# Kernel tuning notes

Measured on AMD Instinct MI355X. Metric: run time of the kernel, lower is better.

## Reference

```python
import jax, jax.numpy as jnp
import numpy as np

B, H, SQ, SKV, D = 4, 16, 1024, 1024, 64


def setup_inputs() -> dict:
    key = jax.random.key(0)
    k1, k2, k3, k4, k5 = jax.random.split(key, 5)
    return {
        "query": jax.random.normal(k1, (B, H, SQ, D), dtype=jnp.float32),
        "keys": jax.random.normal(k2, (B, H, SKV, D), dtype=jnp.float32),
        "values": jax.random.normal(k3, (B, H, SKV, D), dtype=jnp.float32),
        "mask": jax.random.randint(k4, (B, 1, SQ, SKV), 0, 2, dtype=jnp.int32),
        "additional_logits": jax.random.normal(k5, (B, H, SQ, SKV), dtype=jnp.float32),
    }


def reference(query, keys, values, mask, additional_logits):
    # logits = Q K^T + additional_logits, scaled by sqrt(d)
    logits = jnp.einsum("bhqd,bhkd->bhqk", query, keys)
    logits = logits + additional_logits
    logits = logits / jnp.sqrt(jnp.asarray(query.shape[-1], logits.dtype))
    # masked_fill(mask == 0, -1000.0); mask broadcasts over heads
    logits = jnp.where(mask == 0, jnp.asarray(-1000.0, logits.dtype), logits)
    weights = jax.nn.softmax(logits, axis=-1)
    context_vector = jnp.einsum("bhqk,bhkd->bhqd", weights, values)
    return context_vector, weights
```

## Files before the change

kernel.cpp:

```cpp
#include <hip/hip_runtime.h>

#define NB 4
#define NH 16
#define NSQ 1024
#define NSKV 1024
#define ND 64

typedef __attribute__((ext_vector_type(8))) short short8;
typedef __attribute__((ext_vector_type(4))) float f32x4;
typedef __attribute__((ext_vector_type(4))) int int4v;
typedef __attribute__((ext_vector_type(4))) unsigned int uint4v;
typedef __attribute__((ext_vector_type(2))) unsigned int uint2v;

__device__ __forceinline__ unsigned int cvt_pk(float lo, float hi) {
  unsigned int r;
  asm("v_cvt_pk_bf16_f32 %0, %1, %2" : "=v"(r) : "v"(lo), "v"(hi));
  return r;
}
__device__ __forceinline__ unsigned short f2bf(float f) {
  unsigned int u = __float_as_uint(f);
  u += 0x7FFFu + ((u >> 16) & 1u);
  return (unsigned short)(u >> 16);
}
__device__ __forceinline__ float bf2f(unsigned short h) {
  return __uint_as_float(((unsigned int)h) << 16);
}
__device__ __forceinline__ void bar() { __builtin_amdgcn_s_barrier(); }
__device__ __forceinline__ void lgkm0() {
  asm volatile("s_waitcnt lgkmcnt(0)" ::: "memory");
}

__global__ __launch_bounds__(512, 2)
void attn_fused(const float* __restrict__ Q, const float* __restrict__ K,
                const float* __restrict__ V, const int* __restrict__ M,
                const float* __restrict__ A, float* __restrict__ Octx,
                float* __restrict__ Ow)
{
  __shared__ unsigned short Ps[64 * 1024];
  __shared__ __align__(16) unsigned char Stg[18432];
  __shared__ float SumS[64][2];

  const int t  = threadIdx.x;
  const int w  = t >> 6;
  const int l  = t & 63;
  const int lg = l >> 4;
  const int lm = l & 15;
  const int p  = w & 3;
  const int h  = w >> 2;
  const int g  = p * 64 + l;

  const int bid = blockIdx.x;
  const int qt  = bid & 15;
  const int bh  = bid >> 4;
  const int b   = bh >> 4;
  const int q0  = qt * 64;
  const int qw  = q0 + p * 16;
  const int kvb = h * 512;

  const float* Qp = Q + (size_t)bh * NSQ * ND;
  const float* Kp = K + (size_t)bh * NSKV * ND;
  const float* Vp = V + (size_t)bh * NSKV * ND;
  const float* Ap = A + (size_t)bh * NSQ * NSKV;
  const int*   Mp = M + (size_t)b  * NSQ * NSKV;

  unsigned char* KsB = Stg + h * 4096;
  unsigned char* VtB = Stg + 8192 + h * 5120;

  const float C = 0.18033688011112042f;

  short8 qf[2];
  {
    const float* qr = Qp + (size_t)(qw + lm) * ND + lg * 8;
    #pragma unroll
    for (int dc = 0; dc < 2; ++dc) {
      f32x4 x = *(const f32x4*)(qr + dc * 32);
      f32x4 y = *(const f32x4*)(qr + dc * 32 + 4);
      uint4v u;
      u[0] = cvt_pk(x[0], x[1]); u[1] = cvt_pk(x[2], x[3]);
      u[2] = cvt_pk(y[0], y[1]); u[3] = cvt_pk(y[2], y[3]);
      qf[dc] = __builtin_bit_cast(short8, u);
    }
  }

  f32x4 ctx[4];
  #pragma unroll
  for (int i = 0; i < 4; ++i) ctx[i] = (f32x4){0.f, 0.f, 0.f, 0.f};
  float sum = 0.f;

  f32x4 aA[2], aB[2];  int4v mA[2], mB[2];
  f32x4 skA[2], svA[2], skB[2], svB[2];

  auto loadAM = [&](int kv0, f32x4* a, int4v* m) {
    #pragma unroll
    for (int sub = 0; sub < 2; ++sub) {
      size_t off = (size_t)(qw + lm) * NSKV + (kv0 + sub * 16 + lg * 4);
      a[sub] = *(const f32x4*)(Ap + off);
      m[sub] = *(const int4v*)(Mp + off);
    }
  };
  auto issueStage = [&](int kv0, f32x4* sk, f32x4* sv) {
    const float* kb = Kp + (size_t)kv0 * ND;
    const float* vb = Vp + (size_t)kv0 * ND;
    sk[0] = *(const f32x4*)(kb + g * 4);
    sk[1] = *(const f32x4*)(kb + 1024 + g * 4);
    sv[0] = *(const f32x4*)(vb + g * 4);
    sv[1] = *(const f32x4*)(vb + 1024 + g * 4);
  };
  auto writeStage = [&](const f32x4* sk, const f32x4* sv) {
    #pragma unroll
    for (int i = 0; i < 2; ++i) {
      int f = g * 4 + i * 1024;
      int row = f >> 6;
      int cb  = (f & 63) * 2;
      uint2v u;
      u[0] = cvt_pk(sk[i][0], sk[i][1]);
      u[1] = cvt_pk(sk[i][2], sk[i][3]);
      *(uint2v*)(KsB + row * 128 + (cb ^ ((row & 7) << 4))) = u;
      int kv = row, d0 = f & 63;
      #pragma unroll
      for (int j = 0; j < 4; ++j) {
        int d = d0 + j;
        *(unsigned short*)(VtB + d * 80 + ((kv * 2) ^ (((d >> 2) & 3) << 4))) =
            f2bf(sv[i][j]);
      }
    }
  };

  auto chunk = [&](int kv0, const f32x4* a, const int4v* m) {
    const int ksw = (lm & 7) << 4;
    const int vsw = ((lm >> 2) & 3) << 4;
    short8 kf[4];
    #pragma unroll
    for (int sub = 0; sub < 2; ++sub)
      #pragma unroll
      for (int dc = 0; dc < 2; ++dc)
        kf[sub * 2 + dc] = *(const short8*)(
            KsB + (sub * 16 + lm) * 128 + ((dc * 64 + lg * 16) ^ ksw));
    short8 vf[4];
    #pragma unroll
    for (int ds = 0; ds < 4; ++ds)
      vf[ds] = *(const short8*)(VtB + (ds * 16 + lm) * 80 + ((lg * 16) ^ vsw));

    #pragma unroll
    for (int sub = 0; sub < 2; ++sub) {
      f32x4 acc = (f32x4){0.f, 0.f, 0.f, 0.f};
      #pragma unroll
      for (int dc = 0; dc < 2; ++dc)
        acc = __builtin_amdgcn_mfma_f32_16x16x32_bf16(kf[sub * 2 + dc], qf[dc],
                                                      acc, 0, 0, 0);
      float pe[4];
      #pragma unroll
      for (int j = 0; j < 4; ++j) {
        float amc = m[sub][j] ? a[sub][j] * C : -1.8e8f;
        pe[j] = exp2f(fmaf(acc[j], C, amc));
        sum += pe[j];
      }
      uint2v u2;
      u2[0] = cvt_pk(pe[0], pe[1]); u2[1] = cvt_pk(pe[2], pe[3]);
      int colb = (kv0 + sub * 16 + lg * 4) * 2;
      *(uint2v*)((char*)Ps + (p * 16 + lm) * 2048 + (colb ^ (lm << 4))) = u2;
    }
    lgkm0();
    __builtin_amdgcn_sched_barrier(0);
    short8 pf = *(const short8*)((const char*)Ps + (p * 16 + lm) * 2048 +
                                 (((kv0 + lg * 8) * 2) ^ (lm << 4)));
    #pragma unroll
    for (int ds = 0; ds < 4; ++ds)
      ctx[ds] = __builtin_amdgcn_mfma_f32_16x16x32_bf16(pf, vf[ds], ctx[ds], 0, 0, 0);
  };

  issueStage(kvb, skA, svA);
  loadAM(kvb, aA, mA);
  for (int c = 0; c < 16; c += 2) {
    int kv0 = kvb + c * 32;
    bar();
    writeStage(skA, svA);
    issueStage(kv0 + 32, skB, svB);
    loadAM(kv0 + 32, aB, mB);
    lgkm0(); bar();
    chunk(kv0, aA, mA);
    bar();
    writeStage(skB, svB);
    if (c < 14) { issueStage(kv0 + 64, skA, svA); loadAM(kv0 + 64, aA, mA); }
    lgkm0(); bar();
    chunk(kv0 + 32, aB, mB);
  }

  sum += __shfl_xor(sum, 16);
  sum += __shfl_xor(sum, 32);
  if (lg == 0) SumS[p * 16 + lm][h] = sum;
  lgkm0(); bar();

  float (*CtxS)[16][64] = (float(*)[16][64])Stg;
  if (h == 1) {
    #pragma unroll
    for (int ds = 0; ds < 4; ++ds)
      #pragma unroll
      for (int j = 0; j < 4; ++j)
        CtxS[p][lg * 4 + j][ds * 16 + lm] = ctx[ds][j];
  }
  lgkm0(); bar();

  if (h == 0) {
    float rcpj[4];
    #pragma unroll
    for (int j = 0; j < 4; ++j) {
      int r = p * 16 + lg * 4 + j;
      rcpj[j] = 1.0f / (SumS[r][0] + SumS[r][1]);
    }
    #pragma unroll
    for (int ds = 0; ds < 4; ++ds)
      #pragma unroll
      for (int j = 0; j < 4; ++j)
        Octx[((size_t)bh * NSQ + qw + lg * 4 + j) * ND + ds * 16 + lm] =
            (ctx[ds][j] + CtxS[p][lg * 4 + j][ds * 16 + lm]) * rcpj[j];
  }

  float* Owp = Ow + (size_t)bh * NSQ * NSKV + (size_t)qw * NSKV;
  for (int r = 0; r < 16; ++r) {
    float rr = 1.0f / (SumS[p * 16 + r][0] + SumS[p * 16 + r][1]);
    int kv = kvb + l * 8;
    short8 pv = *(const short8*)((const char*)Ps + (p * 16 + r) * 2048 +
                                 ((kv * 2) ^ (r << 4)));
    f32x4 o1, o2;
    o1[0] = bf2f((unsigned short)pv[0]) * rr;
    o1[1] = bf2f((unsigned short)pv[1]) * rr;
    o1[2] = bf2f((unsigned short)pv[2]) * rr;
    o1[3] = bf2f((unsigned short)pv[3]) * rr;
    o2[0] = bf2f((unsigned short)pv[4]) * rr;
    o2[1] = bf2f((unsigned short)pv[5]) * rr;
    o2[2] = bf2f((unsigned short)pv[6]) * rr;
    o2[3] = bf2f((unsigned short)pv[7]) * rr;
    *(f32x4*)&Owp[(size_t)r * NSKV + kv]     = o1;
    *(f32x4*)&Owp[(size_t)r * NSKV + kv + 4] = o2;
  }
}

extern "C" void kernel_launch(void* const* d_in, const int* in_sizes, int n_in,
                              void* d_out, int out_size, void* d_ws, size_t ws_size,
                              hipStream_t stream) {
  const float* Q = (const float*)d_in[0];
  const float* K = (const float*)d_in[1];
  const float* V = (const float*)d_in[2];
  const int*   M = (const int*)d_in[3];
  const float* A = (const float*)d_in[4];
  float* ctx = (float*)d_out;
  float* wts = ctx + (size_t)NB * NH * NSQ * ND;
  dim3 grid(NB * NH * (NSQ / 64));
  attn_fused<<<grid, dim3(512), 0, stream>>>(Q, K, V, M, A, ctx, wts);
}
```

Measured before the change: 205.9 us.

## Split work into 16-row blocks with per-wave private KV staging and quarter KV ranges

Each block now handles 16 query rows with 4 waves, and each wave owns a quarter of the KV range. Every wave stages its own K/V tiles in private LDS, so the main loop needs no block-wide barriers. Shared LDS per block drops sharply, allowing more blocks per CU, and a bid remap interleaves heads. In exchange every K/V tile is reloaded for each 16-row block, four times as often as before, and the partial contexts from four waves must be reduced.

Measured after the change: 243.2 us. 1.18x slower.

```diff
diff --git a/kernel.cpp b/kernel.cpp
--- a/kernel.cpp
+++ b/kernel.cpp
@@ -7,6 +7,7 @@
 #define ND 64
 
 typedef __attribute__((ext_vector_type(8))) short short8;
+typedef __attribute__((ext_vector_type(4))) short short4v;
 typedef __attribute__((ext_vector_type(4))) float f32x4;
 typedef __attribute__((ext_vector_type(4))) int int4v;
 typedef __attribute__((ext_vector_type(4))) unsigned int uint4v;
@@ -25,37 +26,33 @@
 __device__ __forceinline__ float bf2f(unsigned short h) {
   return __uint_as_float(((unsigned int)h) << 16);
 }
-__device__ __forceinline__ void bar() { __builtin_amdgcn_s_barrier(); }
 __device__ __forceinline__ void lgkm0() {
   asm volatile("s_waitcnt lgkmcnt(0)" ::: "memory");
 }
 
-__global__ __launch_bounds__(512, 2)
+__global__ __launch_bounds__(256, 2)
 void attn_fused(const float* __restrict__ Q, const float* __restrict__ K,
                 const float* __restrict__ V, const int* __restrict__ M,
                 const float* __restrict__ A, float* __restrict__ Octx,
                 float* __restrict__ Ow)
 {
-  __shared__ unsigned short Ps[64 * 1024];
-  __shared__ __align__(16) unsigned char Stg[18432];
-  __shared__ float SumS[64][2];
+  __shared__ unsigned short Ps[16 * 1024];
+  __shared__ __align__(16) unsigned short Ks[4][32 * 64];
+  __shared__ __align__(16) unsigned short Vt[4][64 * 40];
+  __shared__ float SumS[16][4];
 
   const int t  = threadIdx.x;
   const int w  = t >> 6;
   const int l  = t & 63;
   const int lg = l >> 4;
   const int lm = l & 15;
-  const int p  = w & 3;
-  const int h  = w >> 2;
-  const int g  = p * 64 + l;
 
   const int bid = blockIdx.x;
-  const int qt  = bid & 15;
-  const int bh  = bid >> 4;
+  const int bh  = (bid & 7) + ((bid >> 9) << 3);
+  const int qt  = (bid >> 3) & 63;
   const int b   = bh >> 4;
-  const int q0  = qt * 64;
-  const int qw  = q0 + p * 16;
-  const int kvb = h * 512;
+  const int q0  = qt * 16;
+  const int kvq = w * 256;
 
   const float* Qp = Q + (size_t)bh * NSQ * ND;
   const float* Kp = K + (size_t)bh * NSKV * ND;
@@ -63,14 +60,14 @@
   const float* Ap = A + (size_t)bh * NSQ * NSKV;
   const int*   Mp = M + (size_t)b  * NSQ * NSKV;
 
-  unsigned char* KsB = Stg + h * 4096;
-  unsigned char* VtB = Stg + 8192 + h * 5120;
+  unsigned short* Ksw = Ks[w];
+  unsigned short* Vtw = Vt[w];
 
   const float C = 0.18033688011112042f;
 
   short8 qf[2];
   {
-    const float* qr = Qp + (size_t)(qw + lm) * ND + lg * 8;
+    const float* qr = Qp + (size_t)(q0 + lm) * ND + lg * 8;
     #pragma unroll
     for (int dc = 0; dc < 2; ++dc) {
       f32x4 x = *(const f32x4*)(qr + dc * 32);
@@ -87,46 +84,43 @@
   for (int i = 0; i < 4; ++i) ctx[i] = (f32x4){0.f, 0.f, 0.f, 0.f};
   float sum = 0.f;
 
+  f32x4 sk[8], sv[8];
   f32x4 aA[2], aB[2];  int4v mA[2], mB[2];
-  f32x4 skA[2], svA[2], skB[2], svB[2];
-
+
+  auto issueStage = [&](int kv0) {
+    const float* kb = Kp + (size_t)kv0 * ND + l * 4;
+    const float* vb = Vp + (size_t)kv0 * ND + l * 4;
+    #pragma unroll
+    for (int i = 0; i < 8; ++i) {
+      sk[i] = *(const f32x4*)(kb + i * 256);
+      sv[i] = *(const f32x4*)(vb + i * 256);
+    }
+  };
   auto loadAM = [&](int kv0, f32x4* a, int4v* m) {
     #pragma unroll
     for (int sub = 0; sub < 2; ++sub) {
-      size_t off = (size_t)(qw + lm) * NSKV + (kv0 + sub * 16 + lg * 4);
+      size_t off = (size_t)(q0 + lm) * NSKV + kv0 + sub * 16 + lg * 4;
       a[sub] = *(const f32x4*)(Ap + off);
       m[sub] = *(const int4v*)(Mp + off);
     }
   };
-  auto issueStage = [&](int kv0, f32x4* sk, f32x4* sv) {
-    const float* kb = Kp + (size_t)kv0 * ND;
-    const float* vb = Vp + (size_t)kv0 * ND;
-    sk[0] = *(const f32x4*)(kb + g * 4);
-    sk[1] = *(const f32x4*)(kb + 1024 + g * 4);
-    sv[0] = *(const f32x4*)(vb + g * 4);
-    sv[1] = *(const f32x4*)(vb + 1024 + g * 4);
-  };
-  auto writeStage = [&](const f32x4* sk, const f32x4* sv) {
-    #pragma unroll
-    for (int i = 0; i < 2; ++i) {
-      int f = g * 4 + i * 1024;
-      int row = f >> 6;
-      int cb  = (f & 63) * 2;
-      uint2v u;
-      u[0] = cvt_pk(sk[i][0], sk[i][1]);
-      u[1] = cvt_pk(sk[i][2], sk[i][3]);
-      *(uint2v*)(KsB + row * 128 + (cb ^ ((row & 7) << 4))) = u;
-      int kv = row, d0 = f & 63;
+  auto writeStage = [&]() {
+    #pragma unroll
+    for (int i = 0; i < 8; ++i) {
+      int row = i * 4 + (l >> 4);
+      uint2v ku;
+      ku[0] = cvt_pk(sk[i][0], sk[i][1]); ku[1] = cvt_pk(sk[i][2], sk[i][3]);
+      *(uint2v*)((char*)Ksw + row * 128 + (((l & 15) * 8) ^ ((row & 7) << 4))) = ku;
       #pragma unroll
       for (int j = 0; j < 4; ++j) {
-        int d = d0 + j;
-        *(unsigned short*)(VtB + d * 80 + ((kv * 2) ^ (((d >> 2) & 3) << 4))) =
-            f2bf(sv[i][j]);
+        int d = (l & 15) * 4 + j;
+        *(unsigned short*)((char*)Vtw + d * 80 +
+                           ((row * 2) ^ (((d >> 2) & 3) << 4))) = f2bf(sv[i][j]);
       }
     }
   };
 
-  auto chunk = [&](int kv0, const f32x4* a, const int4v* m) {
+  auto compute = [&](int kv0, const f32x4* a, const int4v* m) {
     const int ksw = (lm & 7) << 4;
     const int vsw = ((lm >> 2) & 3) << 4;
     short8 kf[4];
@@ -135,11 +129,12 @@
       #pragma unroll
       for (int dc = 0; dc < 2; ++dc)
         kf[sub * 2 + dc] = *(const short8*)(
-            KsB + (sub * 16 + lm) * 128 + ((dc * 64 + lg * 16) ^ ksw));
+            (const char*)Ksw + (sub * 16 + lm) * 128 + ((dc * 64 + lg * 16) ^ ksw));
     short8 vf[4];
     #pragma unroll
     for (int ds = 0; ds < 4; ++ds)
-      vf[ds] = *(const short8*)(VtB + (ds * 16 + lm) * 80 + ((lg * 16) ^ vsw));
+      vf[ds] = *(const short8*)(
+          (const char*)Vtw + (ds * 16 + lm) * 80 + ((lg * 16) ^ vsw));
 
     #pragma unroll
     for (int sub = 0; sub < 2; ++sub) {
@@ -157,82 +152,77 @@
       }
       uint2v u2;
       u2[0] = cvt_pk(pe[0], pe[1]); u2[1] = cvt_pk(pe[2], pe[3]);
-      int colb = (kv0 + sub * 16 + lg * 4) * 2;
-      *(uint2v*)((char*)Ps + (p * 16 + lm) * 2048 + (colb ^ (lm << 4))) = u2;
+      *(uint2v*)((char*)Ps + lm * 2048 +
+                 (((kv0 + sub * 16 + lg * 4) * 2) ^ (lm << 4))) = u2;
     }
     lgkm0();
     __builtin_amdgcn_sched_barrier(0);
-    short8 pf = *(const short8*)((const char*)Ps + (p * 16 + lm) * 2048 +
+    short8 pf = *(const short8*)((const char*)Ps + lm * 2048 +
                                  (((kv0 + lg * 8) * 2) ^ (lm << 4)));
     #pragma unroll
     for (int ds = 0; ds < 4; ++ds)
       ctx[ds] = __builtin_amdgcn_mfma_f32_16x16x32_bf16(pf, vf[ds], ctx[ds], 0, 0, 0);
   };
 
-  issueStage(kvb, skA, svA);
-  loadAM(kvb, aA, mA);
-  for (int c = 0; c < 16; c += 2) {
-    int kv0 = kvb + c * 32;
-    bar();
-    writeStage(skA, svA);
-    issueStage(kv0 + 32, skB, svB);
-    loadAM(kv0 + 32, aB, mB);
-    lgkm0(); bar();
-    chunk(kv0, aA, mA);
-    bar();
-    writeStage(skB, svB);
-    if (c < 14) { issueStage(kv0 + 64, skA, svA); loadAM(kv0 + 64, aA, mA); }
-    lgkm0(); bar();
-    chunk(kv0 + 32, aB, mB);
+  issueStage(kvq);
+  loadAM(kvq, aA, mA);
+  for (int c = 0; c < 8; c += 2) {
+    int kv0 = kvq + c * 32;
+    loadAM(kvq + ((c + 1) & 7) * 32, aB, mB);
+    writeStage();
+    issueStage(kvq + ((c + 1) & 7) * 32);
+    lgkm0();
+    compute(kv0, aA, mA);
+    loadAM(kvq + ((c + 2) & 7) * 32, aA, mA);
+    writeStage();
+    issueStage(kvq + ((c + 2) & 7) * 32);
+    lgkm0();
+    compute(kv0 + 32, aB, mB);
   }
 
   sum += __shfl_xor(sum, 16);
   sum += __shfl_xor(sum, 32);
-  if (lg == 0) SumS[p * 16 + lm][h] = sum;
-  lgkm0(); bar();
-
-  float (*CtxS)[16][64] = (float(*)[16][64])Stg;
-  if (h == 1) {
+  if (l < 16) SumS[l][w] = sum;
+  __syncthreads();
+
+  float (*CtxS)[16][64] = (float(*)[16][64])(&Ks[0][0]);
+  if (w) {
     #pragma unroll
     for (int ds = 0; ds < 4; ++ds)
       #pragma unroll
       for (int j = 0; j < 4; ++j)
-        CtxS[p][lg * 4 + j][ds * 16 + lm] = ctx[ds][j];
-  }
-  lgkm0(); bar();
-
-  if (h == 0) {
-    float rcpj[4];
-    #pragma unroll
-    for (int j = 0; j < 4; ++j) {
-      int r = p * 16 + lg * 4 + j;
-      rcpj[j] = 1.0f / (SumS[r][0] + SumS[r][1]);
-    }
-    #pragma unroll
-    for (int ds = 0; ds < 4; ++ds)
-      #pragma unroll
-      for (int j = 0; j < 4; ++j)
-        Octx[((size_t)bh * NSQ + qw + lg * 4 + j) * ND + ds * 16 + lm] =
-            (ctx[ds][j] + CtxS[p][lg * 4 + j][ds * 16 + lm]) * rcpj[j];
-  }
-
-  float* Owp = Ow + (size_t)bh * NSQ * NSKV + (size_t)qw * NSKV;
+        CtxS[w - 1][lg * 4 + j][ds * 16 + lm] = ctx[ds][j];
+  }
+  __syncthreads();
+
+  float rcpv = 0.f;
+  if (l < 16)
+    rcpv = 1.0f / (SumS[l][0] + SumS[l][1] + SumS[l][2] + SumS[l][3]);
+
+  if (w == 0) {
+    #pragma unroll
+    for (int ds = 0; ds < 4; ++ds)
+      #pragma unroll
+      for (int j = 0; j < 4; ++j) {
+        int qr = lg * 4 + j;
+        float rc = __shfl(rcpv, qr);
+        float v = ctx[ds][j] + CtxS[0][qr][ds * 16 + lm] +
+                  CtxS[1][qr][ds * 16 + lm] + CtxS[2][qr][ds * 16 + lm];
+        Octx[((size_t)bh * NSQ + q0 + qr) * ND + ds * 16 + lm] = v * rc;
+      }
+  }
+
+  float* Owp = Ow + (size_t)bh * NSQ * NSKV + (size_t)q0 * NSKV + kvq;
   for (int r = 0; r < 16; ++r) {
-    float rr = 1.0f / (SumS[p * 16 + r][0] + SumS[p * 16 + r][1]);
-    int kv = kvb + l * 8;
-    short8 pv = *(const short8*)((const char*)Ps + (p * 16 + r) * 2048 +
-                                 ((kv * 2) ^ (r << 4)));
-    f32x4 o1, o2;
-    o1[0] = bf2f((unsigned short)pv[0]) * rr;
-    o1[1] = bf2f((unsigned short)pv[1]) * rr;
-    o1[2] = bf2f((unsigned short)pv[2]) * rr;
-    o1[3] = bf2f((unsigned short)pv[3]) * rr;
-    o2[0] = bf2f((unsigned short)pv[4]) * rr;
-    o2[1] = bf2f((unsigned short)pv[5]) * rr;
-    o2[2] = bf2f((unsigned short)pv[6]) * rr;
-    o2[3] = bf2f((unsigned short)pv[7]) * rr;
-    *(f32x4*)&Owp[(size_t)r * NSKV + kv]     = o1;
-    *(f32x4*)&Owp[(size_t)r * NSKV + kv + 4] = o2;
+    float rr = __shfl(rcpv, r);
+    short4v p = *(const short4v*)((const char*)Ps + r * 2048 +
+                                  (((kvq + l * 4) * 2) ^ (r << 4)));
+    f32x4 o;
+    o[0] = bf2f((unsigned short)p[0]) * rr;
+    o[1] = bf2f((unsigned short)p[1]) * rr;
+    o[2] = bf2f((unsigned short)p[2]) * rr;
+    o[3] = bf2f((unsigned short)p[3]) * rr;
+    *(f32x4*)&Owp[(size_t)r * NSKV + l * 4] = o;
   }
 }
 
@@ -246,6 +236,6 @@
   const float* A = (const float*)d_in[4];
   float* ctx = (float*)d_out;
   float* wts = ctx + (size_t)NB * NH * NSQ * ND;
-  dim3 grid(NB * NH * (NSQ / 64));
-  attn_fused<<<grid, dim3(512), 0, stream>>>(Q, K, V, M, A, ctx, wts);
-}
+  dim3 grid(NB * NH * (NSQ / 16));
+  attn_fused<<<grid, dim3(256), 0, stream>>>(Q, K, V, M, A, ctx, wts);
+}
```

## Shrink blocks to 32 query rows with 256 threads and swizzle block order

Applied to the files above, without the earlier changes.

Each block now handles 32 query rows with 4 waves instead of 64 rows with 8 waves, which halves the P staging buffer in LDS (80KB total) so more blocks can be resident per CU. The K/V staging is reworked so each thread loads four vectors per stage with a tighter V transpose layout. Block IDs are remapped so consecutive blocks interleave batch-heads, and the row-sum reciprocal is computed once per row and broadcast with shuffles. The cost is that each block now reloads and converts the full K and V for only half as many query rows, doubling K/V traffic and staging work.

After: 222.7 us. 1.08x slower.

```diff
diff --git a/kernel.cpp b/kernel.cpp
--- a/kernel.cpp
+++ b/kernel.cpp
@@ -30,32 +30,34 @@
   asm volatile("s_waitcnt lgkmcnt(0)" ::: "memory");
 }
 
-__global__ __launch_bounds__(512, 2)
+__global__ __launch_bounds__(256, 2)
 void attn_fused(const float* __restrict__ Q, const float* __restrict__ K,
                 const float* __restrict__ V, const int* __restrict__ M,
                 const float* __restrict__ A, float* __restrict__ Octx,
                 float* __restrict__ Ow)
 {
-  __shared__ unsigned short Ps[64 * 1024];
-  __shared__ __align__(16) unsigned char Stg[18432];
-  __shared__ float SumS[64][2];
+  __shared__ __align__(16) unsigned char LDS[81920];
+  unsigned short* Ps = (unsigned short*)LDS;
 
   const int t  = threadIdx.x;
   const int w  = t >> 6;
   const int l  = t & 63;
   const int lg = l >> 4;
   const int lm = l & 15;
-  const int p  = w & 3;
-  const int h  = w >> 2;
+  const int p  = w & 1;
+  const int h  = w >> 1;
   const int g  = p * 64 + l;
 
   const int bid = blockIdx.x;
-  const int qt  = bid & 15;
-  const int bh  = bid >> 4;
+  const int y   = bid >> 3;
+  const int qt  = y & 31;
+  const int bh  = (bid & 7) * 8 + (y >> 5);
   const int b   = bh >> 4;
-  const int q0  = qt * 64;
-  const int qw  = q0 + p * 16;
+  const int q0  = qt * 32;
   const int kvb = h * 512;
+
+  unsigned char* KsH = LDS + 65536 + h * 4096;
+  unsigned char* VtH = LDS + 73728 + h * 4096;
 
   const float* Qp = Q + (size_t)bh * NSQ * ND;
   const float* Kp = K + (size_t)bh * NSKV * ND;
@@ -63,21 +65,18 @@
   const float* Ap = A + (size_t)bh * NSQ * NSKV;
   const int*   Mp = M + (size_t)b  * NSQ * NSKV;
 
-  unsigned char* KsB = Stg + h * 4096;
-  unsigned char* VtB = Stg + 8192 + h * 5120;
-
   const float C = 0.18033688011112042f;
 
   short8 qf[2];
   {
-    const float* qr = Qp + (size_t)(qw + lm) * ND + lg * 8;
+    const float* qr = Qp + (size_t)(q0 + p * 16 + lm) * ND + lg * 8;
     #pragma unroll
     for (int dc = 0; dc < 2; ++dc) {
       f32x4 x = *(const f32x4*)(qr + dc * 32);
-      f32x4 y = *(const f32x4*)(qr + dc * 32 + 4);
+      f32x4 y2 = *(const f32x4*)(qr + dc * 32 + 4);
       uint4v u;
       u[0] = cvt_pk(x[0], x[1]); u[1] = cvt_pk(x[2], x[3]);
-      u[2] = cvt_pk(y[0], y[1]); u[3] = cvt_pk(y[2], y[3]);
+      u[2] = cvt_pk(y2[0], y2[1]); u[3] = cvt_pk(y2[2], y2[3]);
       qf[dc] = __builtin_bit_cast(short8, u);
     }
   }
@@ -87,59 +86,58 @@
   for (int i = 0; i < 4; ++i) ctx[i] = (f32x4){0.f, 0.f, 0.f, 0.f};
   float sum = 0.f;
 
+  f32x4 skA[4], svA[4], skB[4], svB[4];
   f32x4 aA[2], aB[2];  int4v mA[2], mB[2];
-  f32x4 skA[2], svA[2], skB[2], svB[2];
-
+
+  auto issueStage = [&](int kv0, f32x4* sk, f32x4* sv) {
+    const float* kb = Kp + (size_t)kv0 * ND + g * 4;
+    const float* vb = Vp + (size_t)kv0 * ND + g * 4;
+    #pragma unroll
+    for (int i = 0; i < 4; ++i) {
+      sk[i] = *(const f32x4*)(kb + i * 512);
+      sv[i] = *(const f32x4*)(vb + i * 512);
+    }
+  };
   auto loadAM = [&](int kv0, f32x4* a, int4v* m) {
     #pragma unroll
     for (int sub = 0; sub < 2; ++sub) {
-      size_t off = (size_t)(qw + lm) * NSKV + (kv0 + sub * 16 + lg * 4);
+      size_t off = (size_t)(q0 + p * 16 + lm) * NSKV + kv0 + sub * 16 + lg * 4;
       a[sub] = *(const f32x4*)(Ap + off);
       m[sub] = *(const int4v*)(Mp + off);
     }
   };
-  auto issueStage = [&](int kv0, f32x4* sk, f32x4* sv) {
-    const float* kb = Kp + (size_t)kv0 * ND;
-    const float* vb = Vp + (size_t)kv0 * ND;
-    sk[0] = *(const f32x4*)(kb + g * 4);
-    sk[1] = *(const f32x4*)(kb + 1024 + g * 4);
-    sv[0] = *(const f32x4*)(vb + g * 4);
-    sv[1] = *(const f32x4*)(vb + 1024 + g * 4);
-  };
   auto writeStage = [&](const f32x4* sk, const f32x4* sv) {
     #pragma unroll
-    for (int i = 0; i < 2; ++i) {
-      int f = g * 4 + i * 1024;
+    for (int i = 0; i < 4; ++i) {
+      int f   = g * 4 + i * 512;
       int row = f >> 6;
-      int cb  = (f & 63) * 2;
-      uint2v u;
-      u[0] = cvt_pk(sk[i][0], sk[i][1]);
-      u[1] = cvt_pk(sk[i][2], sk[i][3]);
-      *(uint2v*)(KsB + row * 128 + (cb ^ ((row & 7) << 4))) = u;
-      int kv = row, d0 = f & 63;
+      int c0  = f & 63;
+      uint2v ku;
+      ku[0] = cvt_pk(sk[i][0], sk[i][1]); ku[1] = cvt_pk(sk[i][2], sk[i][3]);
+      *(uint2v*)(KsH + row * 128 + ((c0 * 2) ^ ((row & 7) << 4))) = ku;
       #pragma unroll
       for (int j = 0; j < 4; ++j) {
-        int d = d0 + j;
-        *(unsigned short*)(VtB + d * 80 + ((kv * 2) ^ (((d >> 2) & 3) << 4))) =
+        int d = c0 + j;
+        *(unsigned short*)(VtH + d * 64 + ((row * 2) ^ (((d >> 1) & 3) << 4))) =
             f2bf(sv[i][j]);
       }
     }
   };
 
-  auto chunk = [&](int kv0, const f32x4* a, const int4v* m) {
+  auto compute = [&](int kv0, const f32x4* a, const int4v* m) {
     const int ksw = (lm & 7) << 4;
-    const int vsw = ((lm >> 2) & 3) << 4;
+    const int vsw = ((lm >> 1) & 3) << 4;
     short8 kf[4];
     #pragma unroll
     for (int sub = 0; sub < 2; ++sub)
       #pragma unroll
       for (int dc = 0; dc < 2; ++dc)
         kf[sub * 2 + dc] = *(const short8*)(
-            KsB + (sub * 16 + lm) * 128 + ((dc * 64 + lg * 16) ^ ksw));
+            KsH + (sub * 16 + lm) * 128 + ((dc * 64 + lg * 16) ^ ksw));
     short8 vf[4];
     #pragma unroll
     for (int ds = 0; ds < 4; ++ds)
-      vf[ds] = *(const short8*)(VtB + (ds * 16 + lm) * 80 + ((lg * 16) ^ vsw));
+      vf[ds] = *(const short8*)(VtH + (ds * 16 + lm) * 64 + ((lg * 16) ^ vsw));
 
     #pragma unroll
     for (int sub = 0; sub < 2; ++sub) {
@@ -157,12 +155,12 @@
       }
       uint2v u2;
       u2[0] = cvt_pk(pe[0], pe[1]); u2[1] = cvt_pk(pe[2], pe[3]);
-      int colb = (kv0 + sub * 16 + lg * 4) * 2;
-      *(uint2v*)((char*)Ps + (p * 16 + lm) * 2048 + (colb ^ (lm << 4))) = u2;
+      *(uint2v*)((char*)Ps + (p * 16 + lm) * 2048 +
+                 (((kv0 + sub * 16 + lg * 4) * 2) ^ (lm << 4))) = u2;
     }
     lgkm0();
     __builtin_amdgcn_sched_barrier(0);
-    short8 pf = *(const short8*)((const char*)Ps + (p * 16 + lm) * 2048 +
+    short8 pf = *(const short8*)((char*)Ps + (p * 16 + lm) * 2048 +
                                  (((kv0 + lg * 8) * 2) ^ (lm << 4)));
     #pragma unroll
     for (int ds = 0; ds < 4; ++ds)
@@ -178,50 +176,51 @@
     issueStage(kv0 + 32, skB, svB);
     loadAM(kv0 + 32, aB, mB);
     lgkm0(); bar();
-    chunk(kv0, aA, mA);
+    compute(kv0, aA, mA);
     bar();
     writeStage(skB, svB);
     if (c < 14) { issueStage(kv0 + 64, skA, svA); loadAM(kv0 + 64, aA, mA); }
     lgkm0(); bar();
-    chunk(kv0 + 32, aB, mB);
+    compute(kv0 + 32, aB, mB);
   }
 
   sum += __shfl_xor(sum, 16);
   sum += __shfl_xor(sum, 32);
-  if (lg == 0) SumS[p * 16 + lm][h] = sum;
-  lgkm0(); bar();
-
-  float (*CtxS)[16][64] = (float(*)[16][64])Stg;
+  __syncthreads();
+
+  float (*CtxS)[64] = (float(*)[64])(LDS + 65536);
+  float (*SumS)[2]  = (float(*)[2])(LDS + 65536 + 8192);
+  if (l < 16) SumS[p * 16 + l][h] = sum;
   if (h == 1) {
     #pragma unroll
     for (int ds = 0; ds < 4; ++ds)
       #pragma unroll
       for (int j = 0; j < 4; ++j)
-        CtxS[p][lg * 4 + j][ds * 16 + lm] = ctx[ds][j];
-  }
-  lgkm0(); bar();
+        CtxS[p * 16 + lg * 4 + j][ds * 16 + lm] = ctx[ds][j];
+  }
+  __syncthreads();
+
+  float rcpv = 0.f;
+  if (l < 16)
+    rcpv = 1.0f / (SumS[p * 16 + l][0] + SumS[p * 16 + l][1]);
 
   if (h == 0) {
-    float rcpj[4];
-    #pragma unroll
-    for (int j = 0; j < 4; ++j) {
-      int r = p * 16 + lg * 4 + j;
-      rcpj[j] = 1.0f / (SumS[r][0] + SumS[r][1]);
-    }
-    #pragma unroll
-    for (int ds = 0; ds < 4; ++ds)
-      #pragma unroll
-      for (int j = 0; j < 4; ++j)
-        Octx[((size_t)bh * NSQ + qw + lg * 4 + j) * ND + ds * 16 + lm] =
-            (ctx[ds][j] + CtxS[p][lg * 4 + j][ds * 16 + lm]) * rcpj[j];
-  }
-
-  float* Owp = Ow + (size_t)bh * NSQ * NSKV + (size_t)qw * NSKV;
+    #pragma unroll
+    for (int ds = 0; ds < 4; ++ds)
+      #pragma unroll
+      for (int j = 0; j < 4; ++j) {
+        int qr = lg * 4 + j;
+        float rc = __shfl(rcpv, qr);
+        float v = ctx[ds][j] + CtxS[p * 16 + qr][ds * 16 + lm];
+        Octx[((size_t)bh * NSQ + q0 + p * 16 + qr) * ND + ds * 16 + lm] = v * rc;
+      }
+  }
+
+  float* Owp = Ow + (size_t)bh * NSQ * NSKV + (size_t)(q0 + p * 16) * NSKV + kvb;
   for (int r = 0; r < 16; ++r) {
-    float rr = 1.0f / (SumS[p * 16 + r][0] + SumS[p * 16 + r][1]);
-    int kv = kvb + l * 8;
-    short8 pv = *(const short8*)((const char*)Ps + (p * 16 + r) * 2048 +
-                                 ((kv * 2) ^ (r << 4)));
+    float rr = __shfl(rcpv, r);
+    short8 pv = *(const short8*)((char*)Ps + (p * 16 + r) * 2048 +
+                                 (((kvb + l * 8) * 2) ^ (r << 4)));
     f32x4 o1, o2;
     o1[0] = bf2f((unsigned short)pv[0]) * rr;
     o1[1] = bf2f((unsigned short)pv[1]) * rr;
@@ -231,8 +230,8 @@
     o2[1] = bf2f((unsigned short)pv[5]) * rr;
     o2[2] = bf2f((unsigned short)pv[6]) * rr;
     o2[3] = bf2f((unsigned short)pv[7]) * rr;
-    *(f32x4*)&Owp[(size_t)r * NSKV + kv]     = o1;
-    *(f32x4*)&Owp[(size_t)r * NSKV + kv + 4] = o2;
+    *(f32x4*)&Owp[(size_t)r * NSKV + l * 8]     = o1;
+    *(f32x4*)&Owp[(size_t)r * NSKV + l * 8 + 4] = o2;
   }
 }
 
@@ -246,6 +245,6 @@
   const float* A = (const float*)d_in[4];
   float* ctx = (float*)d_out;
   float* wts = ctx + (size_t)NB * NH * NSQ * ND;
-  dim3 grid(NB * NH * (NSQ / 64));
-  attn_fused<<<grid, dim3(512), 0, stream>>>(Q, K, V, M, A, ctx, wts);
-}
+  dim3 grid(NB * NH * (NSQ / 32));
+  attn_fused<<<grid, dim3(256), 0, stream>>>(Q, K, V, M, A, ctx, wts);
+}
```

## Ping-pong KV halves between compute and load phases with block remap

Applied to the files above, without the earlier changes.

Restructures the main loop so the two wave halves (h=0 and h=1) alternate roles: while one half computes on its chunk, the other writes staged K/V to LDS and issues the next global loads, with a barrier between each phase. The per-wave staging buffers shrink to a single set, and compute is wrapped in s_setprio to favour MFMA/exp work. The block index is also remapped to interleave batch-heads across consecutive blocks, intended to change L2/XCD locality. The change adds more barriers per iteration and depends on the two halves actually overlapping.

Result: faster. 191.0 us (-7.3%).

```diff
diff --git a/kernel.cpp b/kernel.cpp
--- a/kernel.cpp
+++ b/kernel.cpp
@@ -50,12 +50,15 @@
   const int g  = p * 64 + l;
 
   const int bid = blockIdx.x;
-  const int qt  = bid & 15;
-  const int bh  = bid >> 4;
+  const int y   = bid >> 3;
+  const int qt  = y & 15;
+  const int bh  = (bid & 7) * 8 + (y >> 4);
   const int b   = bh >> 4;
   const int q0  = qt * 64;
-  const int qw  = q0 + p * 16;
   const int kvb = h * 512;
+
+  unsigned char* KsB = Stg + h * 4096;
+  unsigned char* VtB = Stg + 8192 + h * 5120;
 
   const float* Qp = Q + (size_t)bh * NSQ * ND;
   const float* Kp = K + (size_t)bh * NSKV * ND;
@@ -63,21 +66,18 @@
   const float* Ap = A + (size_t)bh * NSQ * NSKV;
   const int*   Mp = M + (size_t)b  * NSQ * NSKV;
 
-  unsigned char* KsB = Stg + h * 4096;
-  unsigned char* VtB = Stg + 8192 + h * 5120;
-
   const float C = 0.18033688011112042f;
 
   short8 qf[2];
   {
-    const float* qr = Qp + (size_t)(qw + lm) * ND + lg * 8;
+    const float* qr = Qp + (size_t)(q0 + p * 16 + lm) * ND + lg * 8;
     #pragma unroll
     for (int dc = 0; dc < 2; ++dc) {
       f32x4 x = *(const f32x4*)(qr + dc * 32);
-      f32x4 y = *(const f32x4*)(qr + dc * 32 + 4);
+      f32x4 y2 = *(const f32x4*)(qr + dc * 32 + 4);
       uint4v u;
       u[0] = cvt_pk(x[0], x[1]); u[1] = cvt_pk(x[2], x[3]);
-      u[2] = cvt_pk(y[0], y[1]); u[3] = cvt_pk(y[2], y[3]);
+      u[2] = cvt_pk(y2[0], y2[1]); u[3] = cvt_pk(y2[2], y2[3]);
       qf[dc] = __builtin_bit_cast(short8, u);
     }
   }
@@ -87,26 +87,26 @@
   for (int i = 0; i < 4; ++i) ctx[i] = (f32x4){0.f, 0.f, 0.f, 0.f};
   float sum = 0.f;
 
+  f32x4 sk[2], sv[2];
   f32x4 aA[2], aB[2];  int4v mA[2], mB[2];
-  f32x4 skA[2], svA[2], skB[2], svB[2];
-
-  auto loadAM = [&](int kv0, f32x4* a, int4v* m) {
+
+  auto issueStage = [&](int c) {
+    int kv0 = kvb + c * 32;
+    const float* kb = Kp + (size_t)kv0 * ND + g * 4;
+    const float* vb = Vp + (size_t)kv0 * ND + g * 4;
+    sk[0] = *(const f32x4*)kb;       sk[1] = *(const f32x4*)(kb + 1024);
+    sv[0] = *(const f32x4*)vb;       sv[1] = *(const f32x4*)(vb + 1024);
+  };
+  auto loadAM = [&](int c, f32x4* a, int4v* m) {
+    int kv0 = kvb + c * 32;
     #pragma unroll
     for (int sub = 0; sub < 2; ++sub) {
-      size_t off = (size_t)(qw + lm) * NSKV + (kv0 + sub * 16 + lg * 4);
+      size_t off = (size_t)(q0 + p * 16 + lm) * NSKV + kv0 + sub * 16 + lg * 4;
       a[sub] = *(const f32x4*)(Ap + off);
       m[sub] = *(const int4v*)(Mp + off);
     }
   };
-  auto issueStage = [&](int kv0, f32x4* sk, f32x4* sv) {
-    const float* kb = Kp + (size_t)kv0 * ND;
-    const float* vb = Vp + (size_t)kv0 * ND;
-    sk[0] = *(const f32x4*)(kb + g * 4);
-    sk[1] = *(const f32x4*)(kb + 1024 + g * 4);
-    sv[0] = *(const f32x4*)(vb + g * 4);
-    sv[1] = *(const f32x4*)(vb + 1024 + g * 4);
-  };
-  auto writeStage = [&](const f32x4* sk, const f32x4* sv) {
+  auto writeStage = [&]() {
     #pragma unroll
     for (int i = 0; i < 2; ++i) {
       int f = g * 4 + i * 1024;
@@ -126,7 +126,8 @@
     }
   };
 
-  auto chunk = [&](int kv0, const f32x4* a, const int4v* m) {
+  auto compute = [&](int c, const f32x4* a, const int4v* m) {
+    int kv0 = kvb + c * 32;
     const int ksw = (lm & 7) << 4;
     const int vsw = ((lm >> 2) & 3) << 4;
     short8 kf[4];
@@ -141,6 +142,7 @@
     for (int ds = 0; ds < 4; ++ds)
       vf[ds] = *(const short8*)(VtB + (ds * 16 + lm) * 80 + ((lg * 16) ^ vsw));
 
+    __builtin_amdgcn_s_setprio(1);
     #pragma unroll
     for (int sub = 0; sub < 2; ++sub) {
       f32x4 acc = (f32x4){0.f, 0.f, 0.f, 0.f};
@@ -157,33 +159,44 @@
       }
       uint2v u2;
       u2[0] = cvt_pk(pe[0], pe[1]); u2[1] = cvt_pk(pe[2], pe[3]);
-      int colb = (kv0 + sub * 16 + lg * 4) * 2;
-      *(uint2v*)((char*)Ps + (p * 16 + lm) * 2048 + (colb ^ (lm << 4))) = u2;
+      *(uint2v*)((char*)Ps + (p * 16 + lm) * 2048 +
+                 (((kv0 + sub * 16 + lg * 4) * 2) ^ (lm << 4))) = u2;
     }
     lgkm0();
     __builtin_amdgcn_sched_barrier(0);
-    short8 pf = *(const short8*)((const char*)Ps + (p * 16 + lm) * 2048 +
+    short8 pf = *(const short8*)((char*)Ps + (p * 16 + lm) * 2048 +
                                  (((kv0 + lg * 8) * 2) ^ (lm << 4)));
     #pragma unroll
     for (int ds = 0; ds < 4; ++ds)
       ctx[ds] = __builtin_amdgcn_mfma_f32_16x16x32_bf16(pf, vf[ds], ctx[ds], 0, 0, 0);
-  };
-
-  issueStage(kvb, skA, svA);
-  loadAM(kvb, aA, mA);
+    __builtin_amdgcn_s_setprio(0);
+  };
+
+  issueStage(0);
+  loadAM(0, aA, mA);
+  if (h == 1) {
+    writeStage();
+    issueStage(1);
+    loadAM(1, aB, mB);
+  }
+  lgkm0(); bar();
+
   for (int c = 0; c < 16; c += 2) {
-    int kv0 = kvb + c * 32;
-    bar();
-    writeStage(skA, svA);
-    issueStage(kv0 + 32, skB, svB);
-    loadAM(kv0 + 32, aB, mB);
-    lgkm0(); bar();
-    chunk(kv0, aA, mA);
-    bar();
-    writeStage(skB, svB);
-    if (c < 14) { issueStage(kv0 + 64, skA, svA); loadAM(kv0 + 64, aA, mA); }
-    lgkm0(); bar();
-    chunk(kv0 + 32, aB, mB);
+    int n1 = (c + 1 > 15) ? 15 : c + 1;
+    int n2 = (c + 2 > 15) ? 15 : c + 2;
+    int n3 = (c + 3 > 15) ? 15 : c + 3;
+    if (h == 0) { writeStage(); issueStage(n1); loadAM(n1, aB, mB); }
+    else        { compute(c, aA, mA); }
+    lgkm0(); bar();
+    if (h == 0) { compute(c, aA, mA); }
+    else        { writeStage(); issueStage(n2); loadAM(n2, aA, mA); }
+    lgkm0(); bar();
+    if (h == 0) { writeStage(); issueStage(n2); loadAM(n2, aA, mA); }
+    else        { compute(c + 1, aB, mB); }
+    lgkm0(); bar();
+    if (h == 0) { compute(c + 1, aB, mB); }
+    else        { writeStage(); issueStage(n3); loadAM(n3, aB, mB); }
+    lgkm0(); bar();
   }
 
   sum += __shfl_xor(sum, 16);
@@ -212,15 +225,15 @@
     for (int ds = 0; ds < 4; ++ds)
       #pragma unroll
       for (int j = 0; j < 4; ++j)
-        Octx[((size_t)bh * NSQ + qw + lg * 4 + j) * ND + ds * 16 + lm] =
+        Octx[((size_t)bh * NSQ + q0 + p * 16 + lg * 4 + j) * ND + ds * 16 + lm] =
             (ctx[ds][j] + CtxS[p][lg * 4 + j][ds * 16 + lm]) * rcpj[j];
   }
 
-  float* Owp = Ow + (size_t)bh * NSQ * NSKV + (size_t)qw * NSKV;
+  float* Owp = Ow + (size_t)bh * NSQ * NSKV + (size_t)(q0 + p * 16) * NSKV;
   for (int r = 0; r < 16; ++r) {
     float rr = 1.0f / (SumS[p * 16 + r][0] + SumS[p * 16 + r][1]);
     int kv = kvb + l * 8;
-    short8 pv = *(const short8*)((const char*)Ps + (p * 16 + r) * 2048 +
+    short8 pv = *(const short8*)((char*)Ps + (p * 16 + r) * 2048 +
                                  ((kv * 2) ^ (r << 4)));
     f32x4 o1, o2;
     o1[0] = bf2f((unsigned short)pv[0]) * rr;
```
